# Optimization experiments

Measured on AMD Instinct MI355X. Metric: run time of the kernel, lower is better.

## Reference

```python
import jax, jax.numpy as jnp
import numpy as np

NUM_HEAD = 8


def setup_inputs() -> dict:
    key = jax.random.key(0)
    k1, k2, k3 = jax.random.split(key, 3)
    B, C, H, W = 8, 512, 32, 32
    x = jax.random.normal(k1, (B, C, H, W), dtype=jnp.float32)
    # 1x1 conv weights stored as plain matrices (out_ch, in_ch)
    Wqkv = jax.random.normal(k2, (3 * C, C), dtype=jnp.float32) * (1.0 / np.sqrt(C))
    Wo = jax.random.normal(k3, (C, C), dtype=jnp.float32) * (1.0 / np.sqrt(C))
    bo = jnp.zeros((C,), dtype=jnp.float32)
    return {"x": x, "Wqkv": Wqkv, "Wo": Wo, "bo": bo}


def reference(x, Wqkv, Wo, bo):
    B, C, H, W = x.shape
    nh = NUM_HEAD
    d = C // nh
    S = H * W
    scale = 1.0 / np.sqrt(d)
    # 1x1 conv == channel matmul: (B,3C,H,W)
    x_ = jnp.einsum('bchw,oc->bohw', x, Wqkv)
    # reshape to (B, nh, 3d, H, W) and chunk along dim 2 (matches torch chunk order)
    qkv = x_.reshape(B, nh, 3 * d, H, W)
    q, k, v = qkv[:, :, :d], qkv[:, :, d:2 * d], qkv[:, :, 2 * d:]
    # flatten heads into batch, spatial into sequence
    q = q.reshape(B * nh, d, S).transpose(0, 2, 1) * scale  # (BH, S, d)
    k = k.reshape(B * nh, d, S)                             # (BH, d, S)
    v = v.reshape(B * nh, d, S).transpose(0, 2, 1)          # (BH, S, d)
    attn = jax.nn.softmax(jnp.matmul(q, k), axis=-1)        # (BH, S, S)
    out = jnp.matmul(attn, v)                               # (BH, S, d)
    result = out.transpose(0, 2, 1).reshape(B, C, H, W)
    # output 1x1 conv with bias + residual
    y = jnp.einsum('bchw,oc->bohw', result, Wo) + bo[None, :, None, None]
    return y + x
```

## Files before the change

### kernel.cpp

```cpp
#include <hip/hip_runtime.h>
#include <hip/hip_bf16.h>

#define C_DIM 512
#define S_DIM 1024
#define NH 8
#define HD 64

typedef __attribute__((ext_vector_type(8))) short bf16x8;
typedef __attribute__((ext_vector_type(8))) unsigned short u16x8;
typedef __attribute__((ext_vector_type(4))) unsigned short u16x4;
typedef __attribute__((ext_vector_type(4))) float f32x4;

__device__ __forceinline__ unsigned short f2b_hw(float f) {
  __hip_bfloat16 h = __float2bfloat16(f);
  return __builtin_bit_cast(unsigned short, h);
}

__device__ __forceinline__ f32x4 mfma16(bf16x8 a, bf16x8 b, f32x4 c) {
  return __builtin_amdgcn_mfma_f32_16x16x32_bf16(a, b, c, 0, 0, 0);
}

__device__ __forceinline__ void gload_lds16(const unsigned short* g, unsigned short* l) {
  __builtin_amdgcn_global_load_lds(
      (const __attribute__((address_space(1))) unsigned int*)g,
      (__attribute__((address_space(3))) unsigned int*)l, 16, 0, 0);
}

__global__ __launch_bounds__(256) void convert_w(
    const float* __restrict__ Wqkv, const float* __restrict__ Wo,
    unsigned short* __restrict__ WqkvB, unsigned short* __restrict__ WoB)
{
  const int i = blockIdx.x * 256 + threadIdx.x;
  const float* src;
  unsigned short* dst;
  int off;
  if (i < 196608) { src = Wqkv; dst = WqkvB; off = i * 4; }
  else            { src = Wo;   dst = WoB;   off = (i - 196608) * 4; }
  const float4 v = *(const float4*)(src + off);
  const u16x4 pk = {f2b_hw(v.x), f2b_hw(v.y), f2b_hw(v.z), f2b_hw(v.w)};
  *(u16x4*)(dst + off) = pk;
}

__global__ __launch_bounds__(256) void xpose_bf16(
    const float* __restrict__ x, unsigned short* __restrict__ xT)
{
  const int b = blockIdx.z, ct = blockIdx.y, st = blockIdx.x;
  const int c0 = ct * 64, s0 = st * 64;
  __shared__ float T[64][65];
  const int tr = threadIdx.x >> 4, tc4 = (threadIdx.x & 15) * 4;
#pragma unroll
  for (int rep = 0; rep < 4; ++rep) {
    const int c = rep * 16 + tr;
    *(float4*)&T[c][tc4] = *(const float4*)(x + ((size_t)(b * C_DIM + c0 + c)) * S_DIM + s0 + tc4);
  }
  __syncthreads();
#pragma unroll
  for (int rep = 0; rep < 4; ++rep) {
    const int s = rep * 16 + tr;
    const u16x4 pk = {f2b_hw(T[tc4 + 0][s]), f2b_hw(T[tc4 + 1][s]),
                      f2b_hw(T[tc4 + 2][s]), f2b_hw(T[tc4 + 3][s])};
    *(u16x4*)(xT + ((size_t)(b * S_DIM + s0 + s)) * C_DIM + c0 + tc4) = pk;
  }
}

template <int MODE>
__global__ __launch_bounds__(256) void mfma_proj(
    const unsigned short* __restrict__ A, const unsigned short* __restrict__ Bm,
    unsigned short* __restrict__ Q, unsigned short* __restrict__ K,
    unsigned short* __restrict__ Vt,
    float* __restrict__ y, const float* __restrict__ bo,
    const float* __restrict__ resid)
{
  const int b = blockIdx.z, ot = blockIdx.y, st = blockIdx.x;
  const int o0 = ot * 128, s0 = st * 128;
  const int tid = threadIdx.x;
  const int w = tid >> 6, lane = tid & 63;
  const int g = lane >> 4, j16 = lane & 15;
  const int wr = w >> 1, wc = w & 1;

  __shared__ __align__(16) unsigned short lds[2048 * 8];
  char* const Al = (char*)lds;
  char* const Bl = (char*)lds + 16384;

  f32x4 acc[4][4];
#pragma unroll
  for (int mt = 0; mt < 4; ++mt)
#pragma unroll
    for (int nt = 0; nt < 4; ++nt) {
      acc[mt][nt].x = 0.f; acc[mt][nt].y = 0.f;
      acc[mt][nt].z = 0.f; acc[mt][nt].w = 0.f;
    }

  for (int k0 = 0; k0 < C_DIM; k0 += 64) {
    __syncthreads();
#pragma unroll
    for (int it = 0; it < 8; ++it) {
      const int chunk = it * 256 + tid;
      const int cid = chunk & 1023;
      const int row = cid >> 3;
      const int colb = (cid & 7) << 4;
      const int srcb = colb ^ ((row & 7) << 4);
      const unsigned short* gp;
      if (it < 4) gp = A + (size_t)(o0 + row) * C_DIM + k0 + (srcb >> 1);
      else        gp = Bm + ((size_t)(b * S_DIM) + s0 + row) * C_DIM + k0 + (srcb >> 1);
      gload_lds16(gp, lds + (size_t)(it * 256 + w * 64) * 8);
    }
    __syncthreads();

#pragma unroll
    for (int ks = 0; ks < 2; ++ks) {
      bf16x8 af[4], bfr[4];
#pragma unroll
      for (int mt = 0; mt < 4; ++mt) {
        const int r = wr * 64 + mt * 16 + j16;
        af[mt] = __builtin_bit_cast(
            bf16x8, *(const u16x8*)(Al + r * 128 + ((ks * 64 + g * 16) ^ ((r & 7) << 4))));
      }
#pragma unroll
      for (int nt = 0; nt < 4; ++nt) {
        const int r = wc * 64 + nt * 16 + j16;
        bfr[nt] = __builtin_bit_cast(
            bf16x8, *(const u16x8*)(Bl + r * 128 + ((ks * 64 + g * 16) ^ ((r & 7) << 4))));
      }
#pragma unroll
      for (int mt = 0; mt < 4; ++mt)
#pragma unroll
        for (int nt = 0; nt < 4; ++nt)
          acc[mt][nt] = mfma16(af[mt], bfr[nt], acc[mt][nt]);
    }
  }

#pragma unroll
  for (int mt = 0; mt < 4; ++mt) {
    const int ob = o0 + wr * 64 + mt * 16 + g * 4;
    if (MODE == 0) {
      const int head = ob / 192, type = (ob % 192) >> 6, d = ob & 63;
      const int bh = b * NH + head;
#pragma unroll
      for (int nt = 0; nt < 4; ++nt) {
        const int s = s0 + wc * 64 + nt * 16 + j16;
        const f32x4 a = acc[mt][nt];
        if (type == 0) {
          const float m = 0.18033688011112042f;
          const u16x4 pk = {f2b_hw(a.x * m), f2b_hw(a.y * m), f2b_hw(a.z * m), f2b_hw(a.w * m)};
          *(u16x4*)(Q + ((size_t)bh * S_DIM + s) * HD + d) = pk;
        } else if (type == 1) {
          const u16x4 pk = {f2b_hw(a.x), f2b_hw(a.y), f2b_hw(a.z), f2b_hw(a.w)};
          *(u16x4*)(K + ((size_t)bh * S_DIM + s) * HD + d) = pk;
        } else {
#pragma unroll
          for (int q = 0; q < 4; ++q)
            Vt[((size_t)bh * HD + d + q) * S_DIM + s] = f2b_hw(a[q]);
        }
      }
    } else {
#pragma unroll
      for (int nt = 0; nt < 4; ++nt) {
        const int s = s0 + wc * 64 + nt * 16 + j16;
#pragma unroll
        for (int q = 0; q < 4; ++q) {
          const int o = ob + q;
          const size_t idx = ((size_t)(b * C_DIM + o)) * S_DIM + s;
          y[idx] = acc[mt][nt][q] + bo[o] + resid[idx];
        }
      }
    }
  }
}

__global__ __launch_bounds__(256) void attn_mfma(
    const unsigned short* __restrict__ Qg, const unsigned short* __restrict__ Kg,
    const unsigned short* __restrict__ Vg, unsigned short* __restrict__ AOt)
{
  const int qb = blockIdx.x;
  const int bh = blockIdx.y;
  const int b = bh >> 3, head = bh & 7;
  const int tid = threadIdx.x;
  const int w = tid >> 6, lane = tid & 63;
  const int g = lane >> 4, j16 = lane & 15;
  const int qw0 = qb * 128 + w * 32;

  __shared__ __align__(16) unsigned short KV[2][2][4096];
  __shared__ __align__(16) unsigned short P_lds[4][32 * 64];

  char* const Pl = (char*)P_lds[w];

  bf16x8 qf[2][2];
#pragma unroll
  for (int nt = 0; nt < 2; ++nt)
#pragma unroll
    for (int ks = 0; ks < 2; ++ks)
      qf[nt][ks] = __builtin_bit_cast(
          bf16x8, *(const u16x8*)(Qg + ((size_t)bh * S_DIM + qw0 + nt * 16 + j16) * HD +
                                  ks * 32 + g * 8));

  const int cid0 = tid;
  const int cid1 = tid + 256;
  auto STAGE = [&](int buf, int k0) {
#pragma unroll
    for (int it = 0; it < 2; ++it) {
      const int cid = it ? cid1 : cid0;
      const int row = cid >> 3;
      const int srcb = ((cid & 7) << 4) ^ ((row & 7) << 4);
      unsigned short* const dst = &KV[buf][0][0] + (size_t)(it * 256 + w * 64) * 8;
      gload_lds16(Kg + ((size_t)bh * S_DIM + k0 + row) * HD + (srcb >> 1), dst);
      gload_lds16(Vg + ((size_t)bh * HD + row) * S_DIM + k0 + (srcb >> 1), dst + 4096);
    }
  };

  f32x4 oacc[4][2];
#pragma unroll
  for (int mt = 0; mt < 4; ++mt)
#pragma unroll
    for (int nt = 0; nt < 2; ++nt) {
      oacc[mt][nt].x = 0.f; oacc[mt][nt].y = 0.f;
      oacc[mt][nt].z = 0.f; oacc[mt][nt].w = 0.f;
    }
  float lsum[2] = {0.f, 0.f};

  STAGE(0, 0);
  __syncthreads();

  for (int kt = 0; kt < 16; ++kt) {
    if (kt < 15) STAGE((kt + 1) & 1, (kt + 1) * 64);

    const char* const Kl = (const char*)KV + (kt & 1) * 16384;
    const char* const Vl = Kl + 8192;

    f32x4 sacc[4][2];
    __builtin_amdgcn_s_setprio(1);
#pragma unroll
    for (int mt = 0; mt < 4; ++mt) {
      const int row = mt * 16 + j16;
      const int sw = (row & 7) << 4;
#pragma unroll
      for (int ks = 0; ks < 2; ++ks) {
        const bf16x8 kf = __builtin_bit_cast(
            bf16x8, *(const u16x8*)(Kl + row * 128 + ((ks * 64 + g * 16) ^ sw)));
        if (ks == 0) {
#pragma unroll
          for (int nt = 0; nt < 2; ++nt) {
            f32x4 z; z.x = 0.f; z.y = 0.f; z.z = 0.f; z.w = 0.f;
            sacc[mt][nt] = mfma16(kf, qf[nt][0], z);
          }
        } else {
#pragma unroll
          for (int nt = 0; nt < 2; ++nt)
            sacc[mt][nt] = mfma16(kf, qf[nt][1], sacc[mt][nt]);
        }
      }
    }
    __builtin_amdgcn_s_setprio(0);

#pragma unroll
    for (int mt = 0; mt < 4; ++mt)
#pragma unroll
      for (int nt = 0; nt < 2; ++nt) {
        f32x4 p;
        p.x = exp2f(sacc[mt][nt].x);
        p.y = exp2f(sacc[mt][nt].y);
        p.z = exp2f(sacc[mt][nt].z);
        p.w = exp2f(sacc[mt][nt].w);
        lsum[nt] += (p.x + p.y) + (p.z + p.w);
        const u16x4 pk = {f2b_hw(p.x), f2b_hw(p.y), f2b_hw(p.z), f2b_hw(p.w)};
        const int qrow = nt * 16 + j16;
        const int kb = (mt * 32 + g * 8) ^ ((qrow & 7) << 4);
        *(u16x4*)(Pl + qrow * 128 + kb) = pk;
      }

    __builtin_amdgcn_s_setprio(1);
#pragma unroll
    for (int kk = 0; kk < 2; ++kk) {
      bf16x8 pf[2];
#pragma unroll
      for (int nt = 0; nt < 2; ++nt) {
        const int qrow = nt * 16 + j16;
        pf[nt] = __builtin_bit_cast(
            bf16x8, *(const u16x8*)(Pl + qrow * 128 + ((kk * 64 + g * 16) ^ ((qrow & 7) << 4))));
      }
#pragma unroll
      for (int mt = 0; mt < 4; ++mt) {
        const int row = mt * 16 + j16;
        const bf16x8 vf = __builtin_bit_cast(
            bf16x8, *(const u16x8*)(Vl + row * 128 + ((kk * 64 + g * 16) ^ ((row & 7) << 4))));
#pragma unroll
        for (int nt = 0; nt < 2; ++nt)
          oacc[mt][nt] = mfma16(vf, pf[nt], oacc[mt][nt]);
      }
    }
    __builtin_amdgcn_s_setprio(0);

    __syncthreads();
  }

#pragma unroll
  for (int nt = 0; nt < 2; ++nt) {
    lsum[nt] += __shfl_xor(lsum[nt], 16);
    lsum[nt] += __shfl_xor(lsum[nt], 32);
    lsum[nt] = 1.f / lsum[nt];
  }

#pragma unroll
  for (int mt = 0; mt < 4; ++mt)
#pragma unroll
    for (int nt = 0; nt < 2; ++nt) {
      const int q = qw0 + nt * 16 + j16;
      const f32x4 a = oacc[mt][nt];
      const float rl = lsum[nt];
      const u16x4 pk = {f2b_hw(a.x * rl), f2b_hw(a.y * rl), f2b_hw(a.z * rl), f2b_hw(a.w * rl)};
      *(u16x4*)(AOt + ((size_t)(b * S_DIM + q)) * C_DIM + head * HD + mt * 16 + g * 4) = pk;
    }
}

extern "C" void kernel_launch(void* const* d_in, const int* in_sizes, int n_in,
                              void* d_out, int out_size, void* d_ws, size_t ws_size,
                              hipStream_t stream) {
  const float* x    = (const float*)d_in[0];
  const float* Wqkv = (const float*)d_in[1];
  const float* Wo   = (const float*)d_in[2];
  const float* bo   = (const float*)d_in[3];
  float* y = (float*)d_out;

  unsigned short* WqkvB = (unsigned short*)d_ws;
  unsigned short* WoB   = WqkvB + 786432;
  unsigned short* xT    = WoB + 262144;
  unsigned short* Q     = xT + 4194304;
  unsigned short* K     = Q + 4194304;
  unsigned short* Vt    = K + 4194304;
  unsigned short* AOt   = Vt + 4194304;

  convert_w<<<dim3(1024), 256, 0, stream>>>(Wqkv, Wo, WqkvB, WoB);
  xpose_bf16<<<dim3(16, 8, 8), 256, 0, stream>>>(x, xT);
  mfma_proj<0><<<dim3(8, 12, 8), 256, 0, stream>>>(WqkvB, xT, Q, K, Vt,
                                                   nullptr, nullptr, nullptr);
  attn_mfma<<<dim3(8, 64), 256, 0, stream>>>(Q, K, Vt, AOt);
  mfma_proj<1><<<dim3(8, 4, 8), 256, 0, stream>>>(WoB, AOt, nullptr, nullptr, nullptr,
                                                  y, bo, x);
}
```

Baseline: 94.01 us.

## Keep softmax probabilities in registers and reorder attention grid

The P tile is no longer written to and re-read from LDS. The exp'd scores are packed straight into the MFMA B-operand registers, and the V reads are split into two 4-element loads whose k-ordering matches the register layout of P. This removes a per-warp LDS round trip and the 16KB P buffer, at the cost of two narrower LDS reads per V fragment. The attention grid is also transposed so that consecutive blocks cover different batch-heads rather than different query blocks of the same head, which changes L2 locality of the K/V data.

```diff
diff --git a/kernel.cpp b/kernel.cpp
--- a/kernel.cpp
+++ b/kernel.cpp
@@ -172,8 +172,8 @@
     const unsigned short* __restrict__ Qg, const unsigned short* __restrict__ Kg,
     const unsigned short* __restrict__ Vg, unsigned short* __restrict__ AOt)
 {
-  const int qb = blockIdx.x;
-  const int bh = blockIdx.y;
+  const int bh = blockIdx.x;
+  const int qb = blockIdx.y;
   const int b = bh >> 3, head = bh & 7;
   const int tid = threadIdx.x;
   const int w = tid >> 6, lane = tid & 63;
@@ -181,9 +181,6 @@
   const int qw0 = qb * 128 + w * 32;
 
   __shared__ __align__(16) unsigned short KV[2][2][4096];
-  __shared__ __align__(16) unsigned short P_lds[4][32 * 64];
-
-  char* const Pl = (char*)P_lds[w];
 
   bf16x8 qf[2][2];
 #pragma unroll
@@ -194,12 +191,10 @@
           bf16x8, *(const u16x8*)(Qg + ((size_t)bh * S_DIM + qw0 + nt * 16 + j16) * HD +
                                   ks * 32 + g * 8));
 
-  const int cid0 = tid;
-  const int cid1 = tid + 256;
   auto STAGE = [&](int buf, int k0) {
 #pragma unroll
     for (int it = 0; it < 2; ++it) {
-      const int cid = it ? cid1 : cid0;
+      const int cid = tid + it * 256;
       const int row = cid >> 3;
       const int srcb = ((cid & 7) << 4) ^ ((row & 7) << 4);
       unsigned short* const dst = &KV[buf][0][0] + (size_t)(it * 256 + w * 64) * 8;
@@ -252,6 +247,7 @@
     }
     __builtin_amdgcn_s_setprio(0);
 
+    u16x4 pf4[2][4];
 #pragma unroll
     for (int mt = 0; mt < 4; ++mt)
 #pragma unroll
@@ -262,30 +258,33 @@
         p.z = exp2f(sacc[mt][nt].z);
         p.w = exp2f(sacc[mt][nt].w);
         lsum[nt] += (p.x + p.y) + (p.z + p.w);
-        const u16x4 pk = {f2b_hw(p.x), f2b_hw(p.y), f2b_hw(p.z), f2b_hw(p.w)};
-        const int qrow = nt * 16 + j16;
-        const int kb = (mt * 32 + g * 8) ^ ((qrow & 7) << 4);
-        *(u16x4*)(Pl + qrow * 128 + kb) = pk;
+        pf4[nt][mt] = u16x4{f2b_hw(p.x), f2b_hw(p.y), f2b_hw(p.z), f2b_hw(p.w)};
       }
 
     __builtin_amdgcn_s_setprio(1);
 #pragma unroll
-    for (int kk = 0; kk < 2; ++kk) {
-      bf16x8 pf[2];
+    for (int ks = 0; ks < 2; ++ks) {
+      bf16x8 pfr[2];
 #pragma unroll
       for (int nt = 0; nt < 2; ++nt) {
-        const int qrow = nt * 16 + j16;
-        pf[nt] = __builtin_bit_cast(
-            bf16x8, *(const u16x8*)(Pl + qrow * 128 + ((kk * 64 + g * 16) ^ ((qrow & 7) << 4))));
+        u16x8 t;
+#pragma unroll
+        for (int e = 0; e < 4; ++e) { t[e] = pf4[nt][2 * ks][e]; t[e + 4] = pf4[nt][2 * ks + 1][e]; }
+        pfr[nt] = __builtin_bit_cast(bf16x8, t);
       }
 #pragma unroll
       for (int mt = 0; mt < 4; ++mt) {
         const int row = mt * 16 + j16;
-        const bf16x8 vf = __builtin_bit_cast(
-            bf16x8, *(const u16x8*)(Vl + row * 128 + ((kk * 64 + g * 16) ^ ((row & 7) << 4))));
+        const int sw = (row & 7) << 4;
+        const u16x4 lo = *(const u16x4*)(Vl + row * 128 + ((ks * 64 + g * 8) ^ sw));
+        const u16x4 hi = *(const u16x4*)(Vl + row * 128 + ((ks * 64 + 32 + g * 8) ^ sw));
+        u16x8 t;
+#pragma unroll
+        for (int e = 0; e < 4; ++e) { t[e] = lo[e]; t[e + 4] = hi[e]; }
+        const bf16x8 vf = __builtin_bit_cast(bf16x8, t);
 #pragma unroll
         for (int nt = 0; nt < 2; ++nt)
-          oacc[mt][nt] = mfma16(vf, pf[nt], oacc[mt][nt]);
+          oacc[mt][nt] = mfma16(vf, pfr[nt], oacc[mt][nt]);
       }
     }
     __builtin_amdgcn_s_setprio(0);
@@ -333,7 +332,7 @@
   xpose_bf16<<<dim3(16, 8, 8), 256, 0, stream>>>(x, xT);
   mfma_proj<0><<<dim3(8, 12, 8), 256, 0, stream>>>(WqkvB, xT, Q, K, Vt,
                                                    nullptr, nullptr, nullptr);
-  attn_mfma<<<dim3(8, 64), 256, 0, stream>>>(Q, K, Vt, AOt);
+  attn_mfma<<<dim3(64, 8), 256, 0, stream>>>(Q, K, Vt, AOt);
   mfma_proj<1><<<dim3(8, 4, 8), 256, 0, stream>>>(WoB, AOt, nullptr, nullptr, nullptr,
                                                   y, bo, x);
 }
```

Result: no change. 92.23 us (-1.9%).
